# Kernel tuning notes

Hardware: AMD Instinct MI355X
Metric: run time of the kernel (lower is better)

The kernel has to match this reference:

```python
import jax, jax.numpy as jnp
import numpy as np

N = 50000      # num_nodes
E = 800000     # num_edges
H = 64         # hidden_dim
L = 4          # num_layers
NH = 4         # num_heads
HD = H // NH   # head_dim


def setup_inputs() -> dict:
    key = jax.random.key(0)
    ks = iter(jax.random.split(key, 64))
    def nrm(shape, s=0.1):
        return jax.random.normal(next(ks), shape, jnp.float32) * s
    inp = dict(
        x=jax.random.normal(next(ks), (N, 4), jnp.float32),
        edge_index=jax.random.randint(next(ks), (2, E), 0, N),
        edge_attr=jax.random.normal(next(ks), (E, 2), jnp.float32),
        in_w=nrm((4, H)), in_b=jnp.zeros((H,), jnp.float32),
        conv_rw1=nrm((L, H + 2, H)), conv_rb1=jnp.zeros((L, H), jnp.float32),
        conv_rw2=nrm((L, H, H)), conv_rb2=jnp.zeros((L, H), jnp.float32),
        conv_iw1=nrm((L, H + 2, H)), conv_ib1=jnp.zeros((L, H), jnp.float32),
        conv_iw2=nrm((L, H, H)), conv_ib2=jnp.zeros((L, H), jnp.float32),
        conv_sw=nrm((L, H, 4 * H)), conv_sb=jnp.zeros((L, 4 * H), jnp.float32),
        att_qw=nrm((L, 4, H)), att_qb=jnp.zeros((L, H), jnp.float32),
        att_kw=nrm((L, 4, H)), att_kb=jnp.zeros((L, H), jnp.float32),
        att_vw=nrm((L, 4, H)), att_vb=jnp.zeros((L, H), jnp.float32),
        att_ow=nrm((L, H, 4)), att_ob=jnp.zeros((L, 4), jnp.float32),
        ln_g=jnp.ones((L, 4), jnp.float32), ln_b=jnp.zeros((L, 4), jnp.float32),
        out_w1=nrm((H, H // 2)), out_b1=jnp.zeros((H // 2,), jnp.float32),
        out_w2=nrm((H // 2, 4)), out_b2=jnp.zeros((4,), jnp.float32),
        res_w=jnp.full((L,), 0.1, jnp.float32),
    )
    return inp


def reference(x, edge_index, edge_attr, in_w, in_b,
              conv_rw1, conv_rb1, conv_rw2, conv_rb2,
              conv_iw1, conv_ib1, conv_iw2, conv_ib2,
              conv_sw, conv_sb,
              att_qw, att_qb, att_kw, att_kb, att_vw, att_vb, att_ow, att_ob,
              ln_g, ln_b, out_w1, out_b1, out_w2, out_b2, res_w):
    n = x.shape[0]
    row, col = edge_index[0], edge_index[1]
    # add_self_loops with edge_attr fill 0 (used only inside the conv)
    loops = jnp.arange(n)
    row_sl = jnp.concatenate([row, loops])
    col_sl = jnp.concatenate([col, loops])
    ea_sl = jnp.concatenate([edge_attr, jnp.zeros((n, 2), edge_attr.dtype)], axis=0)
    deg = jax.ops.segment_sum(jnp.ones((row_sl.shape[0],), x.dtype), col_sl,
                              num_segments=n)[:, None]  # >=1 due to self loops

    h = x @ in_w + in_b  # [N, H]
    for i in range(L):
        residual = x
        # ---- ComplexGraphConv (mean aggregation, source_to_target) ----
        msg_in = jnp.concatenate([h[row_sl], ea_sl], axis=-1)  # [E+N, H+2]
        real = jax.nn.relu(msg_in @ conv_rw1[i] + conv_rb1[i]) @ conv_rw2[i] + conv_rb2[i]
        imag = jax.nn.relu(msg_in @ conv_iw1[i] + conv_ib1[i]) @ conv_iw2[i] + conv_ib2[i]
        mag = jnp.sqrt(real * real + imag * imag)
        phase = jnp.arctan2(imag, real + 1e-8)
        msg = jnp.concatenate([real, imag, mag, phase], axis=-1)  # [E+N, 4H]
        agg = jax.ops.segment_sum(msg, col_sl, num_segments=n) / deg
        h4 = agg + (h @ conv_sw[i] + conv_sb[i])  # [N, 4H]
        x4 = h4[:, :4]
        # ---- ComplexGraphAttention (global edge softmax per head) ----
        Q = (x4 @ att_qw[i] + att_qb[i]).reshape(n, NH, HD)
        K = (x4 @ att_kw[i] + att_kb[i]).reshape(n, NH, HD)
        V = (x4 @ att_vw[i] + att_vb[i]).reshape(n, NH, HD)
        scores = jnp.einsum('ehd,ehd->eh', Q[row], K[col]) / np.sqrt(HD).astype(x.dtype)
        w = jax.nn.softmax(scores, axis=0)  # softmax over ALL edges (dim=0)
        att = jax.ops.segment_sum(w[:, :, None] * V[row], col,
                                  num_segments=n).reshape(n, NH * HD)
        x4 = (att @ att_ow[i] + att_ob[i]) + x4  # out_proj + residual (dropout=eval)
        # ---- LayerNorm over last dim (4) ----
        mu = x4.mean(-1, keepdims=True)
        var = x4.var(-1, keepdims=True)
        x4 = (x4 - mu) / jnp.sqrt(var + 1e-5) * ln_g[i] + ln_b[i]
        x = x4 + residual * res_w[i]
        h = x @ in_w + in_b
    pred = jnp.tanh(jax.nn.relu(h @ out_w1 + out_b1) @ out_w2 + out_b2) * 0.3
    return pred
```

## Files before the change

kernel.cpp:

```cpp
#include <hip/hip_runtime.h>
#include <hip/hip_bf16.h>
#include <hip/hip_fp16.h>

#define N_NODES 50000
#define N_EDGES 800000
#define BUCKET 64
#define EDGE_TB 3125
#define COPY_NB 196
#define DST_PER_XCD 6250

__device__ __forceinline__ float rdlane(float v, int k) {
    return __uint_as_float(__builtin_amdgcn_readlane(__float_as_uint(v), k));
}
template <int CTRL>
__device__ __forceinline__ float dpp_addf(float v) {
    int x = __builtin_amdgcn_update_dpp(0, __float_as_int(v), CTRL, 0xF, 0xF, true);
    return v + __int_as_float(x);
}
#define DPP_QX1  0xB1
#define DPP_QX2  0x4E
#define DPP_HM   0x141
#define DPP_RM   0x140
#define DPP_ROR4 0x124
#define DPP_ROR8 0x128
__device__ __forceinline__ float dpp_sum16(float v) {
    v = dpp_addf<DPP_QX1>(v);
    v = dpp_addf<DPP_QX2>(v);
    v = dpp_addf<DPP_HM>(v);
    v = dpp_addf<DPP_RM>(v);
    return v;
}
__device__ __forceinline__ void bsum4(float& v0, float& v1, float& v2, float& v3) {
    #pragma unroll
    for (int m = 1; m < 64; m <<= 1) {
        v0 += __shfl_xor(v0, m);
        v1 += __shfl_xor(v1, m);
        v2 += __shfl_xor(v2, m);
        v3 += __shfl_xor(v3, m);
    }
}

__global__ void k_setup(const float* __restrict__ x, unsigned* __restrict__ cntC,
                        float4* __restrict__ xcur,
                        const int* __restrict__ row, const int* __restrict__ col,
                        const float* __restrict__ ea, uint2* __restrict__ colEA,
                        const float* __restrict__ qw, const float* __restrict__ qb,
                        const float* __restrict__ kw, const float* __restrict__ kb,
                        const float* __restrict__ vw, const float* __restrict__ vb,
                        const float* __restrict__ ow,
                        const float* __restrict__ in_w, const float* __restrict__ in_b,
                        const float* __restrict__ rw1all, const float* __restrict__ rb1all,
                        const float* __restrict__ swall,
                        float* __restrict__ cst, float* __restrict__ cstV,
                        float* __restrict__ cstM) {
    int tid = threadIdx.x;
    int bid = blockIdx.x;
    if (bid < 8 * EDGE_TB) {
        int filt = bid & 7;
        int e = (bid >> 3) * 256 + tid;
        if (e < N_EDGES) {
            int c = col[e];
            if (c / DST_PER_XCD == filt) {
                unsigned slot = atomicAdd(&cntC[c], 1u);
                float2 e2 = ((const float2*)ea)[e];
                __half2 h2 = __floats2half2_rn(e2.x, e2.y);
                colEA[(size_t)c * BUCKET + slot] =
                    make_uint2(*reinterpret_cast<unsigned*>(&h2), (unsigned)row[e]);
            }
        }
        return;
    }
    if (bid < 8 * EDGE_TB + COPY_NB) {
        int n = (bid - 8 * EDGE_TB) * 256 + tid;
        if (n < N_NODES) xcur[n] = ((const float4*)x)[n];
        return;
    }
    int pb = bid - (8 * EDGE_TB + COPY_NB);
    int m = tid;
    if (m >= 64) return;
    int d = m & 15;
    if (pb < 4) {
        int L = pb;
        const float* qwl = qw + L * 256; const float* kwl = kw + L * 256;
        const float* qbl = qb + L * 64;  const float* kbl = kb + L * 64;
        float qa[4], ka[4];
        #pragma unroll
        for (int a = 0; a < 4; a++) { qa[a] = qwl[a * 64 + m]; ka[a] = kwl[a * 64 + m]; }
        float qbm = qbl[m], kbm = kbl[m];
        float vals[25];
        int idx = 0;
        #pragma unroll
        for (int a = 0; a < 4; a++)
            #pragma unroll
            for (int b = 0; b < 4; b++) vals[idx++] = qa[a] * ka[b];
        #pragma unroll
        for (int a = 0; a < 4; a++) vals[idx++] = qa[a] * kbm;
        #pragma unroll
        for (int b = 0; b < 4; b++) vals[idx++] = qbm * ka[b];
        vals[24] = qbm * kbm;
        #pragma unroll
        for (int i = 0; i < 25; i++) {
            float v = vals[i];
            v += __shfl_xor(v, 1); v += __shfl_xor(v, 2);
            v += __shfl_xor(v, 4); v += __shfl_xor(v, 8);
            vals[i] = v;
        }
        if (d == 0) {
            float* out = cst + L * 128 + (m >> 4) * 32;
            #pragma unroll
            for (int i = 0; i < 25; i++) out[i] = vals[i] * 0.25f;
        }
    } else if (pb < 8) {
        int L = pb - 4;
        int h = m >> 4;
        const float* vwl = vw + L * 256;
        const float* vbl = vb + L * 64;
        float4 owv = ((const float4*)(ow + L * 256))[m];
        float vals[20];
        #pragma unroll
        for (int a = 0; a < 4; a++) {
            float v = vwl[a * 64 + m];
            vals[a * 4 + 0] = v * owv.x; vals[a * 4 + 1] = v * owv.y;
            vals[a * 4 + 2] = v * owv.z; vals[a * 4 + 3] = v * owv.w;
        }
        float b = vbl[m];
        vals[16] = b * owv.x; vals[17] = b * owv.y; vals[18] = b * owv.z; vals[19] = b * owv.w;
        #pragma unroll
        for (int i = 0; i < 20; i++) {
            float v = vals[i];
            v += __shfl_xor(v, 1); v += __shfl_xor(v, 2);
            v += __shfl_xor(v, 4); v += __shfl_xor(v, 8);
            vals[i] = v;
        }
        if (d == 0) {
            float* out = cstV + L * 128 + h * 32;
            #pragma unroll
            for (int i = 0; i < 20; i++) out[i] = vals[i];
        }
    } else {
        int L = pb - 8;
        const float* rw1 = rw1all + L * 66 * 64;
        const float* rb1 = rb1all + L * 64;
        const float* sw  = swall + L * 64 * 256;
        float* M = cstM + L * 384;
        float bacc = rb1[m];
        float w0 = 0.f, w1 = 0.f, w2 = 0.f, w3 = 0.f;
        for (int k = 0; k < 64; k++) {
            float r = rw1[k * 64 + m];
            bacc += in_b[k] * r;
            w0 += in_w[k] * r;
            w1 += in_w[64 + k] * r;
            w2 += in_w[128 + k] * r;
            w3 += in_w[192 + k] * r;
        }
        M[m * 4 + 0] = w0; M[m * 4 + 1] = w1; M[m * 4 + 2] = w2; M[m * 4 + 3] = w3;
        M[256 + m] = bacc;
        if (m < 16) {
            int a = m >> 2, o = m & 3;
            float sacc = 0.f;
            for (int k = 0; k < 64; k++) sacc += in_w[a * 64 + k] * sw[k * 256 + o];
            M[320 + m] = sacc;
        }
        if (m < 4) {
            float sacc = 0.f;
            for (int k = 0; k < 64; k++) sacc += in_b[k] * sw[k * 256 + m];
            M[336 + m] = sacc;
        }
    }
}

__global__ void k61(const float* __restrict__ att16, const float* __restrict__ sumexpP,
                    const float4* __restrict__ x4b, const float* __restrict__ ob,
                    const float* __restrict__ g, const float* __restrict__ bb,
                    const float* __restrict__ resw, float4* __restrict__ xcur) {
    int tid = threadIdx.x;
    int wid = (blockIdx.x * blockDim.x + tid) >> 6;
    int lane = tid & 63;
    int n0 = wid * 4;
    if (n0 >= N_NODES) return;
    float4 zp = ((const float4*)sumexpP)[lane];
    bsum4(zp.x, zp.y, zp.z, zp.w);
    int hh = (lane & 15) >> 2;
    float z = (hh == 0) ? zp.x : (hh == 1) ? zp.y : (hh == 2) ? zp.z : zp.w;
    float ob0 = ob[0], ob1 = ob[1], ob2 = ob[2], ob3 = ob[3];
    float g0 = g[0], g1 = g[1], g2 = g[2], g3 = g[3];
    float bb0 = bb[0], bb1 = bb[1], bb2 = bb[2], bb3 = bb[3];
    float rw = resw[0];
    #pragma unroll
    for (int i = 0; i < 4; i++) {
        int n = n0 + i;
        float a = 0.f;
        if (n < N_NODES && lane < 16) a = att16[n * 16 + lane] / z;
        a = dpp_addf<DPP_ROR4>(a);
        a = dpp_addf<DPP_ROR8>(a);
        float y0 = rdlane(a, 0), y1 = rdlane(a, 1), y2 = rdlane(a, 2), y3 = rdlane(a, 3);
        if (n < N_NODES) {
            float4 x4v = x4b[n];
            y0 += ob0 + x4v.x; y1 += ob1 + x4v.y;
            y2 += ob2 + x4v.z; y3 += ob3 + x4v.w;
            float mu = 0.25f * (y0 + y1 + y2 + y3);
            float d0 = y0 - mu, d1 = y1 - mu, d2 = y2 - mu, d3 = y3 - mu;
            float var = 0.25f * (d0 * d0 + d1 * d1 + d2 * d2 + d3 * d3);
            float rs = rsqrtf(var + 1e-5f);
            float4 xold = xcur[n];
            float nn0 = d0 * rs * g0 + bb0 + xold.x * rw;
            float nn1 = d1 * rs * g1 + bb1 + xold.y * rw;
            float nn2 = d2 * rs * g2 + bb2 + xold.z * rw;
            float nn3 = d3 * rs * g3 + bb3 + xold.w * rw;
            if (lane == 0) xcur[n] = make_float4(nn0, nn1, nn2, nn3);
        }
    }
}

__global__ void k23b(const unsigned* __restrict__ cntC, const uint2* __restrict__ colEA,
                     const float4* __restrict__ xcur, const float* __restrict__ rw1,
                     const float* __restrict__ rw2, const float* __restrict__ cstM,
                     const float* __restrict__ rb2, const float* __restrict__ sb,
                     float4* __restrict__ x4b, float* __restrict__ sumexpP) {
    __shared__ float s_rw2[64][4];
    __shared__ float s_weff[64][4];
    __shared__ float s_w1[128];
    __shared__ float s_beff[64];
    __shared__ float s_sw16[16];
    __shared__ float s_sbe[4];
    __shared__ float4 s_x[16][16];
    __shared__ float2 s_e[16][16];
    int tid = threadIdx.x;
    { int r = tid >> 2, cc = tid & 3; s_rw2[r][cc] = rw2[r * 64 + cc]; s_weff[r][cc] = cstM[tid]; }
    if (tid < 128) s_w1[tid] = rw1[64 * 64 + tid];
    if (tid < 64) s_beff[tid] = cstM[256 + tid];
    if (tid < 16) s_sw16[tid] = cstM[320 + tid];
    if (tid < 4)  s_sbe[tid]  = cstM[336 + tid];
    if (blockIdx.x == 0) sumexpP[tid] = 0.f;
    __syncthreads();
    int l16 = tid & 15, grp = tid >> 4;
    float wf[4][4], bfr[4], w1a[4], w1b[4], wr2r[4][4];
    #pragma unroll
    for (int j = 0; j < 4; j++) {
        int ch = l16 * 4 + j;
        #pragma unroll
        for (int a = 0; a < 4; a++) wf[j][a] = s_weff[ch][a];
        bfr[j] = s_beff[ch];
        w1a[j] = s_w1[ch];
        w1b[j] = s_w1[64 + ch];
        #pragma unroll
        for (int o = 0; o < 4; o++) wr2r[j][o] = s_rw2[ch][o];
    }
    int c = blockIdx.x * 16 + grp;
    float4 xc = xcur[c];
    int cnt = (int)cntC[c];
    const uint2* rowE = colEA + (size_t)c * BUCKET;
    int items = cnt + 1;
    float a0 = 0.f, a1 = 0.f, a2 = 0.f, a3 = 0.f;
    for (int base = 0; base < items; base += 16) {
        int it = base + l16;
        float4 xr = make_float4(0.f, 0.f, 0.f, 0.f);
        float2 ef2 = make_float2(0.f, 0.f);
        if (it < items) {
            if (it == 0) {
                xr = xc;
            } else {
                uint2 er = rowE[it - 1];
                xr = xcur[er.y];
                __half2 eh = *reinterpret_cast<const __half2*>(&er.x);
                ef2 = __half22float2(eh);
            }
        }
        s_x[grp][l16] = xr;
        s_e[grp][l16] = ef2;
        int lim = items - base; if (lim > 16) lim = 16;
        for (int q = 0; q < lim; q++) {
            float4 xq = s_x[grp][q];
            float2 eq = s_e[grp][q];
            #pragma unroll
            for (int j = 0; j < 4; j++) {
                float tk = bfr[j] + xq.x * wf[j][0] + xq.y * wf[j][1]
                         + xq.z * wf[j][2] + xq.w * wf[j][3];
                float pre = tk + eq.x * w1a[j] + eq.y * w1b[j];
                float rr = fmaxf(pre, 0.f);
                a0 += rr * wr2r[j][0]; a1 += rr * wr2r[j][1];
                a2 += rr * wr2r[j][2]; a3 += rr * wr2r[j][3];
            }
        }
    }
    a0 = dpp_sum16(a0); a1 = dpp_sum16(a1); a2 = dpp_sum16(a2); a3 = dpp_sum16(a3);
    if (l16 == 0) {
        float idg = 1.f / (float)(cnt + 1);
        float b0 = xc.x * s_sw16[0] + xc.y * s_sw16[4] + xc.z * s_sw16[8]  + xc.w * s_sw16[12] + s_sbe[0];
        float b1 = xc.x * s_sw16[1] + xc.y * s_sw16[5] + xc.z * s_sw16[9]  + xc.w * s_sw16[13] + s_sbe[1];
        float b2 = xc.x * s_sw16[2] + xc.y * s_sw16[6] + xc.z * s_sw16[10] + xc.w * s_sw16[14] + s_sbe[2];
        float b3 = xc.x * s_sw16[3] + xc.y * s_sw16[7] + xc.z * s_sw16[11] + xc.w * s_sw16[15] + s_sbe[3];
        x4b[c] = make_float4(a0 * idg + b0 + rb2[0] + sb[0],
                             a1 * idg + b1 + rb2[1] + sb[1],
                             a2 * idg + b2 + rb2[2] + sb[2],
                             a3 * idg + b3 + rb2[3] + sb[3]);
    }
}

__global__ void k5_att(const unsigned* __restrict__ cntC, const uint2* __restrict__ colEA,
                       const float4* __restrict__ x4b, const float* __restrict__ cst,
                       const float* __restrict__ cstV, float* __restrict__ att16,
                       float* __restrict__ sumexpP) {
    __shared__ float s_cst[128];
    __shared__ float s_cstV[128];
    __shared__ float zs[16][4];
    int tid = threadIdx.x;
    if (tid < 128) { s_cst[tid] = cst[tid]; s_cstV[tid] = cstV[tid]; }
    __syncthreads();
    int l16 = tid & 15, grp = tid >> 4;
    int c = blockIdx.x * 16 + grp;
    float4 xc = x4b[c];
    float gh[4][4], bh[4];
    #pragma unroll
    for (int h = 0; h < 4; h++) {
        const float* C = s_cst + h * 32;
        gh[h][0] = xc.x * C[0]  + xc.y * C[1]  + xc.z * C[2]  + xc.w * C[3]  + C[16];
        gh[h][1] = xc.x * C[4]  + xc.y * C[5]  + xc.z * C[6]  + xc.w * C[7]  + C[17];
        gh[h][2] = xc.x * C[8]  + xc.y * C[9]  + xc.z * C[10] + xc.w * C[11] + C[18];
        gh[h][3] = xc.x * C[12] + xc.y * C[13] + xc.z * C[14] + xc.w * C[15] + C[19];
        bh[h]    = C[20] * xc.x + C[21] * xc.y + C[22] * xc.z + C[23] * xc.w + C[24];
    }
    int cnt = (int)cntC[c];
    const unsigned* rowY = (const unsigned*)(colEA + (size_t)c * BUCKET);
    float S00 = 0.f, S01 = 0.f, S02 = 0.f, S03 = 0.f;
    float S10 = 0.f, S11 = 0.f, S12 = 0.f, S13 = 0.f;
    float S20 = 0.f, S21 = 0.f, S22 = 0.f, S23 = 0.f;
    float S30 = 0.f, S31 = 0.f, S32 = 0.f, S33 = 0.f;
    float z0 = 0.f, z1 = 0.f, z2 = 0.f, z3 = 0.f;
    for (int base = 0; base < cnt; base += 16) {
        int it = base + l16;
        bool act = it < cnt;
        float4 xr = make_float4(0.f, 0.f, 0.f, 0.f);
        if (act) xr = x4b[rowY[2 * it + 1]];
        float actf = act ? 1.f : 0.f;
        {
            float s = xr.x * gh[0][0] + xr.y * gh[0][1] + xr.z * gh[0][2] + xr.w * gh[0][3] + bh[0];
            float ex = __expf(s) * actf;
            z0 += ex; S00 += ex * xr.x; S01 += ex * xr.y; S02 += ex * xr.z; S03 += ex * xr.w;
        }
        {
            float s = xr.x * gh[1][0] + xr.y * gh[1][1] + xr.z * gh[1][2] + xr.w * gh[1][3] + bh[1];
            float ex = __expf(s) * actf;
            z1 += ex; S10 += ex * xr.x; S11 += ex * xr.y; S12 += ex * xr.z; S13 += ex * xr.w;
        }
        {
            float s = xr.x * gh[2][0] + xr.y * gh[2][1] + xr.z * gh[2][2] + xr.w * gh[2][3] + bh[2];
            float ex = __expf(s) * actf;
            z2 += ex; S20 += ex * xr.x; S21 += ex * xr.y; S22 += ex * xr.z; S23 += ex * xr.w;
        }
        {
            float s = xr.x * gh[3][0] + xr.y * gh[3][1] + xr.z * gh[3][2] + xr.w * gh[3][3] + bh[3];
            float ex = __expf(s) * actf;
            z3 += ex; S30 += ex * xr.x; S31 += ex * xr.y; S32 += ex * xr.z; S33 += ex * xr.w;
        }
    }
    S00 = dpp_sum16(S00); S01 = dpp_sum16(S01); S02 = dpp_sum16(S02); S03 = dpp_sum16(S03);
    S10 = dpp_sum16(S10); S11 = dpp_sum16(S11); S12 = dpp_sum16(S12); S13 = dpp_sum16(S13);
    S20 = dpp_sum16(S20); S21 = dpp_sum16(S21); S22 = dpp_sum16(S22); S23 = dpp_sum16(S23);
    S30 = dpp_sum16(S30); S31 = dpp_sum16(S31); S32 = dpp_sum16(S32); S33 = dpp_sum16(S33);
    z0 = dpp_sum16(z0); z1 = dpp_sum16(z1); z2 = dpp_sum16(z2); z3 = dpp_sum16(z3);
    int h = l16 >> 2, a = l16 & 3;
    float Sa0 = (h == 0) ? S00 : (h == 1) ? S10 : (h == 2) ? S20 : S30;
    float Sa1 = (h == 0) ? S01 : (h == 1) ? S11 : (h == 2) ? S21 : S31;
    float Sa2 = (h == 0) ? S02 : (h == 1) ? S12 : (h == 2) ? S22 : S32;
    float Sa3 = (h == 0) ? S03 : (h == 1) ? S13 : (h == 2) ? S23 : S33;
    float zh  = (h == 0) ? z0  : (h == 1) ? z1  : (h == 2) ? z2  : z3;
    const float* V = s_cstV + h * 32;
    float my = Sa0 * V[0 * 4 + a] + Sa1 * V[1 * 4 + a] + Sa2 * V[2 * 4 + a] + Sa3 * V[3 * 4 + a]
             + zh * V[16 + a];
    att16[c * 16 + l16] = my;
    if (a == 0) zs[grp][h] = zh;
    __syncthreads();
    if (tid < 4) {
        float acc = 0.f;
        #pragma unroll
        for (int q = 0; q < 16; q++) acc += zs[q][tid];
        atomicAdd(&sumexpP[((blockIdx.x & 63) << 2) + tid], acc);
    }
}

__global__ void k6pred(const float* __restrict__ att16, const float* __restrict__ sumexpP,
                       const float4* __restrict__ x4b, const float* __restrict__ ob,
                       const float* __restrict__ g, const float* __restrict__ bb,
                       const float* __restrict__ resw, const float4* __restrict__ xcur,
                       const float* __restrict__ in_w, const float* __restrict__ in_b,
                       const float* __restrict__ w1, const float* __restrict__ b1,
                       const float* __restrict__ w2, const float* __restrict__ b2,
                       float* __restrict__ out) {
    int tid = threadIdx.x;
    int node = (blockIdx.x * blockDim.x + tid) >> 6;
    int lane = tid & 63;
    if (node >= N_NODES) return;
    float4 zp = ((const float4*)sumexpP)[lane];
    bsum4(zp.x, zp.y, zp.z, zp.w);
    int hh = (lane & 15) >> 2;
    float z = (hh == 0) ? zp.x : (hh == 1) ? zp.y : (hh == 2) ? zp.z : zp.w;
    float a = 0.f;
    if (lane < 16) a = att16[node * 16 + lane] / z;
    a = dpp_addf<DPP_ROR4>(a);
    a = dpp_addf<DPP_ROR8>(a);
    float y0 = rdlane(a, 0), y1 = rdlane(a, 1), y2 = rdlane(a, 2), y3 = rdlane(a, 3);
    float4 x4v = x4b[node];
    y0 += ob[0] + x4v.x; y1 += ob[1] + x4v.y;
    y2 += ob[2] + x4v.z; y3 += ob[3] + x4v.w;
    float mu = 0.25f * (y0 + y1 + y2 + y3);
    float d0 = y0 - mu, d1 = y1 - mu, d2 = y2 - mu, d3 = y3 - mu;
    float var = 0.25f * (d0 * d0 + d1 * d1 + d2 * d2 + d3 * d3);
    float rs = rsqrtf(var + 1e-5f);
    float4 xold = xcur[node];
    float rw = resw[0];
    float n0 = d0 * rs * g[0] + bb[0] + xold.x * rw;
    float n1 = d1 * rs * g[1] + bb[1] + xold.y * rw;
    float n2 = d2 * rs * g[2] + bb[2] + xold.z * rw;
    float n3 = d3 * rs * g[3] + bb[3] + xold.w * rw;
    float hv = in_b[lane] + n0 * in_w[lane] + n1 * in_w[64 + lane]
             + n2 * in_w[128 + lane] + n3 * in_w[192 + lane];
    int j2 = lane & 31;
    float m = b1[j2];
    for (int k = 0; k < 64; k++) m += rdlane(hv, k) * w1[k * 32 + j2];
    m = fmaxf(m, 0.f);
    float4 w2v = ((const float4*)w2)[j2];
    float v0 = m * w2v.x, v1 = m * w2v.y, v2 = m * w2v.z, v3 = m * w2v.w;
    bsum4(v0, v1, v2, v3);
    float o0 = tanhf(0.5f * v0 + b2[0]) * 0.3f;
    float o1 = tanhf(0.5f * v1 + b2[1]) * 0.3f;
    float o2 = tanhf(0.5f * v2 + b2[2]) * 0.3f;
    float o3 = tanhf(0.5f * v3 + b2[3]) * 0.3f;
    if (lane == 0) ((float4*)out)[node] = make_float4(o0, o1, o2, o3);
}

extern "C" void kernel_launch(void* const* d_in, const int* in_sizes, int n_in,
                              void* d_out, int out_size, void* d_ws, size_t ws_size,
                              hipStream_t stream) {
    const float* x        = (const float*)d_in[0];
    const int*   ei       = (const int*)d_in[1];
    const float* ea       = (const float*)d_in[2];
    const float* in_w     = (const float*)d_in[3];
    const float* in_b     = (const float*)d_in[4];
    const float* conv_rw1 = (const float*)d_in[5];
    const float* conv_rb1 = (const float*)d_in[6];
    const float* conv_rw2 = (const float*)d_in[7];
    const float* conv_rb2 = (const float*)d_in[8];
    const float* conv_sw  = (const float*)d_in[13];
    const float* conv_sb  = (const float*)d_in[14];
    const float* att_qw   = (const float*)d_in[15];
    const float* att_qb   = (const float*)d_in[16];
    const float* att_kw   = (const float*)d_in[17];
    const float* att_kb   = (const float*)d_in[18];
    const float* att_vw   = (const float*)d_in[19];
    const float* att_vb   = (const float*)d_in[20];
    const float* att_ow   = (const float*)d_in[21];
    const float* att_ob   = (const float*)d_in[22];
    const float* ln_g     = (const float*)d_in[23];
    const float* ln_b     = (const float*)d_in[24];
    const float* out_w1   = (const float*)d_in[25];
    const float* out_b1   = (const float*)d_in[26];
    const float* out_w2   = (const float*)d_in[27];
    const float* out_b2   = (const float*)d_in[28];
    const float* res_w    = (const float*)d_in[29];

    const int* row = ei;
    const int* col = ei + N_EDGES;

    char* ws = (char*)d_ws;
    size_t off = 0;
    auto alloc = [&](size_t bytes) -> void* {
        void* p = ws + off;
        off = (off + bytes + 255) & ~(size_t)255;
        return p;
    };
    unsigned* cntC     = (unsigned*)alloc(N_NODES * 4);
    uint2*    colEA    = (uint2*)alloc((size_t)N_NODES * BUCKET * 8);
    float*    att16    = (float*)alloc((size_t)N_NODES * 16 * 4);
    float4*   x4b      = (float4*)alloc((size_t)N_NODES * 16);
    float4*   xcur     = (float4*)alloc((size_t)N_NODES * 16);
    float*    cst      = (float*)alloc(4 * 128 * 4);
    float*    cstV     = (float*)alloc(4 * 128 * 4);
    float*    cstM     = (float*)alloc(4 * 384 * 4);
    float*    sumexpP  = (float*)alloc(64 * 4 * 4);

    dim3 b256(256);
    int grpBlocks   = (N_NODES + 15) / 16;
    int nodeBlocks4 = (N_NODES + 15) / 16;

    hipMemsetAsync(cntC, 0, N_NODES * 4, stream);
    k_setup<<<8 * EDGE_TB + COPY_NB + 12, b256, 0, stream>>>(
        x, cntC, xcur, row, col, ea, colEA,
        att_qw, att_qb, att_kw, att_kb, att_vw, att_vb, att_ow,
        in_w, in_b, conv_rw1, conv_rb1, conv_sw,
        cst, cstV, cstM);

    for (int i = 0; i < 4; i++) {
        const float* rw1 = conv_rw1 + i * 66 * 64;
        const float* rw2 = conv_rw2 + i * 64 * 64;
        const float* rb2 = conv_rb2 + i * 64;
        const float* sbl = conv_sb + i * 256;

        if (i > 0) {
            k61<<<nodeBlocks4, b256, 0, stream>>>(att16, sumexpP, x4b,
                                                  att_ob + (i - 1) * 4, ln_g + (i - 1) * 4,
                                                  ln_b + (i - 1) * 4, res_w + (i - 1),
                                                  xcur);
        }
        k23b<<<grpBlocks, b256, 0, stream>>>(cntC, colEA, xcur, rw1, rw2,
                                             cstM + i * 384, rb2, sbl, x4b, sumexpP);
        k5_att<<<grpBlocks, b256, 0, stream>>>(cntC, colEA, x4b, cst + i * 128,
                                               cstV + i * 128, att16, sumexpP);
    }
    k6pred<<<(N_NODES + 3) / 4, b256, 0, stream>>>(att16, sumexpP, x4b, att_ob + 12, ln_g + 12,
                                            ln_b + 12, res_w + 3, xcur, in_w, in_b,
                                            out_w1, out_b1, out_w2, out_b2, (float*)d_out);
}
```

Baseline: 399.6 us.

## Remap attention kernel to one wavefront per node with per-head lanes

The attention aggregation kernel now gives each destination node a full 64-lane wavefront instead of a 16-lane group. Each lane handles one head and one edge slot, so it keeps 5 accumulators instead of 20, and the sums are combined with xor shuffles. This cuts register pressure and exp work per lane, which should raise occupancy and parallelism. The cost is four times as many blocks, repeated x4b row gathers across the 4 head lanes, and more shuffle reductions. The edge-bucketing setup also switches its col, row and edge_attr reads to nontemporal loads.

Measured after the change: 466.9 us. 1.17x slower.

```diff
diff --git a/kernel.cpp b/kernel.cpp
--- a/kernel.cpp
+++ b/kernel.cpp
@@ -59,13 +59,15 @@
         int filt = bid & 7;
         int e = (bid >> 3) * 256 + tid;
         if (e < N_EDGES) {
-            int c = col[e];
+            int c = __builtin_nontemporal_load(&col[e]);
             if (c / DST_PER_XCD == filt) {
                 unsigned slot = atomicAdd(&cntC[c], 1u);
-                float2 e2 = ((const float2*)ea)[e];
-                __half2 h2 = __floats2half2_rn(e2.x, e2.y);
+                float ex_ = __builtin_nontemporal_load(&ea[2 * e]);
+                float ey_ = __builtin_nontemporal_load(&ea[2 * e + 1]);
+                int r = __builtin_nontemporal_load(&row[e]);
+                __half2 h2 = __floats2half2_rn(ex_, ey_);
                 colEA[(size_t)c * BUCKET + slot] =
-                    make_uint2(*reinterpret_cast<unsigned*>(&h2), (unsigned)row[e]);
+                    make_uint2(*reinterpret_cast<unsigned*>(&h2), (unsigned)r);
             }
         }
         return;
@@ -303,78 +305,54 @@
                        float* __restrict__ sumexpP) {
     __shared__ float s_cst[128];
     __shared__ float s_cstV[128];
-    __shared__ float zs[16][4];
+    __shared__ float zs[4][4];
     int tid = threadIdx.x;
     if (tid < 128) { s_cst[tid] = cst[tid]; s_cstV[tid] = cstV[tid]; }
     __syncthreads();
-    int l16 = tid & 15, grp = tid >> 4;
-    int c = blockIdx.x * 16 + grp;
+    int lane = tid & 63;
+    int wv = tid >> 6;
+    int c = (blockIdx.x * blockDim.x + tid) >> 6;
+    int h = lane & 3;
+    int itl = lane >> 2;
     float4 xc = x4b[c];
-    float gh[4][4], bh[4];
-    #pragma unroll
-    for (int h = 0; h < 4; h++) {
-        const float* C = s_cst + h * 32;
-        gh[h][0] = xc.x * C[0]  + xc.y * C[1]  + xc.z * C[2]  + xc.w * C[3]  + C[16];
-        gh[h][1] = xc.x * C[4]  + xc.y * C[5]  + xc.z * C[6]  + xc.w * C[7]  + C[17];
-        gh[h][2] = xc.x * C[8]  + xc.y * C[9]  + xc.z * C[10] + xc.w * C[11] + C[18];
-        gh[h][3] = xc.x * C[12] + xc.y * C[13] + xc.z * C[14] + xc.w * C[15] + C[19];
-        bh[h]    = C[20] * xc.x + C[21] * xc.y + C[22] * xc.z + C[23] * xc.w + C[24];
-    }
+    const float* C = s_cst + h * 32;
+    float g0 = xc.x * C[0]  + xc.y * C[1]  + xc.z * C[2]  + xc.w * C[3]  + C[16];
+    float g1 = xc.x * C[4]  + xc.y * C[5]  + xc.z * C[6]  + xc.w * C[7]  + C[17];
+    float g2 = xc.x * C[8]  + xc.y * C[9]  + xc.z * C[10] + xc.w * C[11] + C[18];
+    float g3 = xc.x * C[12] + xc.y * C[13] + xc.z * C[14] + xc.w * C[15] + C[19];
+    float base = C[20] * xc.x + C[21] * xc.y + C[22] * xc.z + C[23] * xc.w + C[24];
     int cnt = (int)cntC[c];
     const unsigned* rowY = (const unsigned*)(colEA + (size_t)c * BUCKET);
-    float S00 = 0.f, S01 = 0.f, S02 = 0.f, S03 = 0.f;
-    float S10 = 0.f, S11 = 0.f, S12 = 0.f, S13 = 0.f;
-    float S20 = 0.f, S21 = 0.f, S22 = 0.f, S23 = 0.f;
-    float S30 = 0.f, S31 = 0.f, S32 = 0.f, S33 = 0.f;
-    float z0 = 0.f, z1 = 0.f, z2 = 0.f, z3 = 0.f;
-    for (int base = 0; base < cnt; base += 16) {
-        int it = base + l16;
+    float S0 = 0.f, S1 = 0.f, S2 = 0.f, S3 = 0.f, z = 0.f;
+    for (int bb = 0; bb < cnt; bb += 16) {
+        int it = bb + itl;
         bool act = it < cnt;
         float4 xr = make_float4(0.f, 0.f, 0.f, 0.f);
         if (act) xr = x4b[rowY[2 * it + 1]];
-        float actf = act ? 1.f : 0.f;
-        {
-            float s = xr.x * gh[0][0] + xr.y * gh[0][1] + xr.z * gh[0][2] + xr.w * gh[0][3] + bh[0];
-            float ex = __expf(s) * actf;
-            z0 += ex; S00 += ex * xr.x; S01 += ex * xr.y; S02 += ex * xr.z; S03 += ex * xr.w;
-        }
-        {
-            float s = xr.x * gh[1][0] + xr.y * gh[1][1] + xr.z * gh[1][2] + xr.w * gh[1][3] + bh[1];
-            float ex = __expf(s) * actf;
-            z1 += ex; S10 += ex * xr.x; S11 += ex * xr.y; S12 += ex * xr.z; S13 += ex * xr.w;
-        }
-        {
-            float s = xr.x * gh[2][0] + xr.y * gh[2][1] + xr.z * gh[2][2] + xr.w * gh[2][3] + bh[2];
-            float ex = __expf(s) * actf;
-            z2 += ex; S20 += ex * xr.x; S21 += ex * xr.y; S22 += ex * xr.z; S23 += ex * xr.w;
-        }
-        {
-            float s = xr.x * gh[3][0] + xr.y * gh[3][1] + xr.z * gh[3][2] + xr.w * gh[3][3] + bh[3];
-            float ex = __expf(s) * actf;
-            z3 += ex; S30 += ex * xr.x; S31 += ex * xr.y; S32 += ex * xr.z; S33 += ex * xr.w;
-        }
-    }
-    S00 = dpp_sum16(S00); S01 = dpp_sum16(S01); S02 = dpp_sum16(S02); S03 = dpp_sum16(S03);
-    S10 = dpp_sum16(S10); S11 = dpp_sum16(S11); S12 = dpp_sum16(S12); S13 = dpp_sum16(S13);
-    S20 = dpp_sum16(S20); S21 = dpp_sum16(S21); S22 = dpp_sum16(S22); S23 = dpp_sum16(S23);
-    S30 = dpp_sum16(S30); S31 = dpp_sum16(S31); S32 = dpp_sum16(S32); S33 = dpp_sum16(S33);
-    z0 = dpp_sum16(z0); z1 = dpp_sum16(z1); z2 = dpp_sum16(z2); z3 = dpp_sum16(z3);
-    int h = l16 >> 2, a = l16 & 3;
-    float Sa0 = (h == 0) ? S00 : (h == 1) ? S10 : (h == 2) ? S20 : S30;
-    float Sa1 = (h == 0) ? S01 : (h == 1) ? S11 : (h == 2) ? S21 : S31;
-    float Sa2 = (h == 0) ? S02 : (h == 1) ? S12 : (h == 2) ? S22 : S32;
-    float Sa3 = (h == 0) ? S03 : (h == 1) ? S13 : (h == 2) ? S23 : S33;
-    float zh  = (h == 0) ? z0  : (h == 1) ? z1  : (h == 2) ? z2  : z3;
-    const float* V = s_cstV + h * 32;
-    float my = Sa0 * V[0 * 4 + a] + Sa1 * V[1 * 4 + a] + Sa2 * V[2 * 4 + a] + Sa3 * V[3 * 4 + a]
-             + zh * V[16 + a];
-    att16[c * 16 + l16] = my;
-    if (a == 0) zs[grp][h] = zh;
+        float s = xr.x * g0 + xr.y * g1 + xr.z * g2 + xr.w * g3 + base;
+        float ex = __expf(s) * (act ? 1.f : 0.f);
+        z += ex; S0 += ex * xr.x; S1 += ex * xr.y; S2 += ex * xr.z; S3 += ex * xr.w;
+    }
+    #pragma unroll
+    for (int m = 4; m < 64; m <<= 1) {
+        S0 += __shfl_xor(S0, m); S1 += __shfl_xor(S1, m);
+        S2 += __shfl_xor(S2, m); S3 += __shfl_xor(S3, m);
+        z  += __shfl_xor(z, m);
+    }
+    if (lane < 4) zs[wv][lane] = z;
+    int ho = lane >> 2, a = lane & 3;
+    float T0 = __shfl(S0, ho), T1 = __shfl(S1, ho);
+    float T2 = __shfl(S2, ho), T3 = __shfl(S3, ho);
+    float tz = __shfl(z, ho);
+    if (lane < 16) {
+        const float* V = s_cstV + ho * 32;
+        float my = T0 * V[0 * 4 + a] + T1 * V[1 * 4 + a] + T2 * V[2 * 4 + a] + T3 * V[3 * 4 + a]
+                 + tz * V[16 + a];
+        att16[c * 16 + lane] = my;
+    }
     __syncthreads();
     if (tid < 4) {
-        float acc = 0.f;
-        #pragma unroll
-        for (int q = 0; q < 16; q++) acc += zs[q][tid];
+        float acc = zs[0][tid] + zs[1][tid] + zs[2][tid] + zs[3][tid];
         atomicAdd(&sumexpP[((blockIdx.x & 63) << 2) + tid], acc);
     }
 }
@@ -481,6 +459,7 @@
 
     dim3 b256(256);
     int grpBlocks   = (N_NODES + 15) / 16;
+    int attBlocks   = (N_NODES + 3) / 4;
     int nodeBlocks4 = (N_NODES + 15) / 16;
 
     hipMemsetAsync(cntC, 0, N_NODES * 4, stream);
@@ -504,7 +483,7 @@
         }
         k23b<<<grpBlocks, b256, 0, stream>>>(cntC, colEA, xcur, rw1, rw2,
                                              cstM + i * 384, rb2, sbl, x4b, sumexpP);
-        k5_att<<<grpBlocks, b256, 0, stream>>>(cntC, colEA, x4b, cst + i * 128,
+        k5_att<<<attBlocks, b256, 0, stream>>>(cntC, colEA, x4b, cst + i * 128,
                                                cstV + i * 128, att16, sumexpP);
     }
     k6pred<<<(N_NODES + 3) / 4, b256, 0, stream>>>(att16, sumexpP, x4b, att_ob + 12, ln_g + 12,
```
